# Performance work log

Hardware: AMD Instinct MI355X
Metric: run time of the kernel (lower is better)

The kernel has to match this reference:

```python
import jax, jax.numpy as jnp
import numpy as np

B, HG, WG, D, NH, K = 4, 32, 32, 768, 12, 7
HD = D // NH  # 64


def _neigh_idx(H, W, k):
    # NATTEN semantics: 7x7 window centered at the query, shifted (clamped)
    # at borders so every query has exactly k*k neighbors.
    si = np.clip(np.arange(H) - k // 2, 0, H - k)  # [H] window row starts
    sj = np.clip(np.arange(W) - k // 2, 0, W - k)  # [W] window col starts
    ri = si[:, None] + np.arange(k)[None, :]       # [H, k]
    cj = sj[:, None] + np.arange(k)[None, :]       # [W, k]
    idx = ri[:, None, :, None] * W + cj[None, :, None, :]  # [H, W, k, k]
    return jnp.asarray(idx.reshape(H * W, k * k), dtype=jnp.int32)


def setup_inputs() -> dict:
    key = jax.random.key(0)
    ks = jax.random.split(key, 3)
    s = D ** -0.5
    return {
        "x": jax.random.normal(ks[0], (B, HG * WG, D), dtype=jnp.float32),
        "qkv_w": jax.random.normal(ks[1], (3 * D, D), dtype=jnp.float32) * s,
        "qkv_b": jnp.zeros((3 * D,), dtype=jnp.float32),
        "proj_w": jax.random.normal(ks[2], (D, D), dtype=jnp.float32) * s,
        "proj_b": jnp.zeros((D,), dtype=jnp.float32),
    }


def reference(x, qkv_w, qkv_b, proj_w, proj_b):
    b, n, d = x.shape  # n == HG*WG
    idx = _neigh_idx(HG, WG, K)  # [n, K*K] flat neighbor token indices

    qkv = x @ qkv_w.T + qkv_b                      # [b, n, 3d]
    q, k, v = jnp.split(qkv, 3, axis=-1)
    q = q.reshape(b, n, NH, HD) * (HD ** -0.5)     # [b, n, h, hd]
    k = k.reshape(b, n, NH, HD)
    v = v.reshape(b, n, NH, HD)

    kn = jnp.take(k, idx, axis=1)                  # [b, n, 49, h, hd]
    vn = jnp.take(v, idx, axis=1)                  # [b, n, 49, h, hd]

    scores = jnp.einsum('bnhd,bnkhd->bnhk', q, kn)  # [b, n, h, 49]
    attn = jax.nn.softmax(scores, axis=-1)
    out = jnp.einsum('bnhk,bnkhd->bnhd', attn, vn).reshape(b, n, d)
    return out @ proj_w.T + proj_b
```

## Files before the change

kernel.cpp:

```cpp
#include <hip/hip_runtime.h>


typedef __bf16 bf16x8 __attribute__((ext_vector_type(8)));
typedef short s16x4 __attribute__((ext_vector_type(4)));
typedef float f32x4 __attribute__((ext_vector_type(4)));

__device__ __forceinline__ unsigned short f2bf(float f) {
  unsigned u = __float_as_uint(f);
  u += 0x7fffu + ((u >> 16) & 1u);
  return (unsigned short)(u >> 16);
}

template <typename T>
__device__ __forceinline__ void gld_lds16(const T* g, T* l) {
  __builtin_amdgcn_global_load_lds((const __attribute__((address_space(1))) void*)g,
                                   (__attribute__((address_space(3))) void*)l, 16, 0, 0);
}

__global__ void cvt_kernel(const float* __restrict__ x, const float* __restrict__ w1,
                           const float* __restrict__ w2, unsigned short* __restrict__ xo,
                           unsigned short* __restrict__ w1o, unsigned short* __restrict__ w2o) {
  const int n1 = 4096 * 768 / 4;
  const int n2 = 2304 * 768 / 4;
  const int n3 = 768 * 768 / 4;
  int i = blockIdx.x * 256 + threadIdx.x;
  float4 v;
  unsigned short* dst;
  int o;
  if (i < n1) {
    o = i; v = ((const float4*)x)[o]; dst = xo;
  } else if (i < n1 + n2) {
    o = i - n1; v = ((const float4*)w1)[o]; dst = w1o;
  } else if (i < n1 + n2 + n3) {
    o = i - n1 - n2; v = ((const float4*)w2)[o]; dst = w2o;
  } else {
    return;
  }
  ushort4 r;
  r.x = f2bf(v.x); r.y = f2bf(v.y); r.z = f2bf(v.z); r.w = f2bf(v.w);
  ((ushort4*)dst)[o] = r;
}

template <int MODE, int BM, int BN>
__global__ __launch_bounds__(256) void gemm_bt(const unsigned short* __restrict__ A,
                                               const unsigned short* __restrict__ Bm,
                                               const float* __restrict__ bias,
                                               unsigned short* __restrict__ obf,
                                               unsigned short* __restrict__ vtout,
                                               float* __restrict__ of32,
                                               int M, int N, int Kd) {
  constexpr int RA = BM / 64, RB = BN / 64;
  constexpr int MI = BM / 32, NI = BN / 32;
  __shared__ __align__(16) unsigned short sA[2][BM * 32];
  __shared__ __align__(16) unsigned short sB[2][BN * 32];
  const int tid = threadIdx.x;
  const int lane = tid & 63;
  const int wv = tid >> 6;

  constexpr int HX = (MODE == 0) ? 9 : 6;
  constexpr int HY = (MODE == 0) ? 8 : 16;
  const int lin = blockIdx.y * gridDim.x + blockIdx.x;
  const int xcd = lin & 7, rrr = lin >> 3;
  const int bx = (xcd & 1) * HX + rrr % HX;
  const int by = (xcd >> 1) * HY + rrr / HX;
  const int m0 = by * BM, n0 = bx * BN;

  const int wrow = (wv >> 1) * (BM / 2), wcol = (wv & 1) * (BN / 2);
  const int lr = lane & 15, lq = lane >> 4;
  const int rchunk = (lq ^ ((lr >> 1) & 3)) * 8;

  f32x4 acc[MI][NI] = {};

  const int schunk = ((tid & 3) ^ ((tid >> 3) & 3)) * 8;
  const unsigned short* gA = A + (size_t)(m0 + (tid >> 2)) * Kd + schunk;
  const unsigned short* gB = Bm + (size_t)(n0 + (tid >> 2)) * Kd + schunk;

#pragma unroll
  for (int r = 0; r < RA; ++r) gld_lds16(gA + (size_t)(r * 64) * Kd, &sA[0][r * 2048 + tid * 8]);
#pragma unroll
  for (int r = 0; r < RB; ++r) gld_lds16(gB + (size_t)(r * 64) * Kd, &sB[0][r * 2048 + tid * 8]);
  __syncthreads();

  int cur = 0;
  for (int k0 = 0; k0 < Kd; k0 += 32) {
    const int nxt = k0 + 32;
    if (nxt < Kd) {
      unsigned short* dA = sA[cur ^ 1];
      unsigned short* dB = sB[cur ^ 1];
#pragma unroll
      for (int r = 0; r < RA; ++r) gld_lds16(gA + (size_t)(r * 64) * Kd + nxt, dA + r * 2048 + tid * 8);
#pragma unroll
      for (int r = 0; r < RB; ++r) gld_lds16(gB + (size_t)(r * 64) * Kd + nxt, dB + r * 2048 + tid * 8);
    }
    const unsigned short* cA = sA[cur];
    const unsigned short* cB = sB[cur];
    bf16x8 af[MI], bfr[NI];
#pragma unroll
    for (int t = 0; t < MI; ++t) af[t] = *(const bf16x8*)(cA + (wrow + t * 16 + lr) * 32 + rchunk);
#pragma unroll
    for (int t = 0; t < NI; ++t) bfr[t] = *(const bf16x8*)(cB + (wcol + t * 16 + lr) * 32 + rchunk);
#pragma unroll
    for (int im = 0; im < MI; ++im)
#pragma unroll
      for (int in = 0; in < NI; ++in)
        acc[im][in] = __builtin_amdgcn_mfma_f32_16x16x32_bf16(af[im], bfr[in], acc[im][in], 0, 0, 0);
    __syncthreads();
    cur ^= 1;
  }

  if (MODE == 0) {
    const int sidx = n0 / 768;
    if (sidx == 2) {
#pragma unroll
      for (int im = 0; im < MI; ++im) {
#pragma unroll
        for (int in = 0; in < NI; ++in) {
          int gn = n0 + wcol + in * 16 + lr;
          int rem = gn - 1536;
          int hh = rem >> 6, dd = gn & 63;
          float bsv = bias[gn];
          int gm0 = m0 + wrow + im * 16 + lq * 4;
          ushort4 pk;
          pk.x = f2bf(acc[im][in][0] + bsv);
          pk.y = f2bf(acc[im][in][1] + bsv);
          pk.z = f2bf(acc[im][in][2] + bsv);
          pk.w = f2bf(acc[im][in][3] + bsv);
          *(ushort4*)(vtout + (size_t)(hh * 64 + dd) * 4096 + gm0) = pk;
        }
      }
    } else {
      const float scale = (sidx == 0) ? 0.18033688f : 1.0f;
#pragma unroll
      for (int im = 0; im < MI; ++im) {
#pragma unroll
        for (int in = 0; in < NI; ++in) {
          int gn = n0 + wcol + in * 16 + lr;
          int rem = gn - sidx * 768;
          int hh = rem >> 6, dd = gn & 63;
          float bsv = bias[gn];
#pragma unroll
          for (int r = 0; r < 4; ++r) {
            int gm = m0 + wrow + im * 16 + lq * 4 + r;
            float val = (acc[im][in][r] + bsv) * scale;
            obf[((size_t)(sidx * 12 + hh) * 4096 + gm) * 64 + dd] = f2bf(val);
          }
        }
      }
    }
  } else {
#pragma unroll
    for (int im = 0; im < MI; ++im) {
#pragma unroll
      for (int in = 0; in < NI; ++in) {
        int gn = n0 + wcol + in * 16 + lr;
        float bsv = bias[gn];
#pragma unroll
        for (int r = 0; r < 4; ++r) {
          int gm = m0 + wrow + im * 16 + lq * 4 + r;
          of32[(size_t)gm * N + gn] = acc[im][in][r] + bsv;
        }
      }
    }
  }
}

__global__ __launch_bounds__(256, 3) void natten_kernel(const unsigned short* __restrict__ qkvt,
                                                        unsigned short* __restrict__ aout) {
  __shared__ __align__(16) unsigned short sKV[256 * 64];
  const int h = blockIdx.x, ip = blockIdx.y, b = blockIdx.z;
  const int i0 = ip * 2;
  const int tid = threadIdx.x, lane = tid & 63, wv = tid >> 6;
  const int lg = lane >> 4, lm = lane & 15;
  int si0 = i0 - 3; si0 = si0 < 0 ? 0 : si0; if (si0 > 25) si0 = 25;
  const int gb = b * 1024;
  const unsigned short* Qg = qkvt + ((size_t)h * 4096 + gb + i0 * 32) * 64;
  const unsigned short* Kg = qkvt + ((size_t)(12 + h) * 4096 + gb) * 64;
  const unsigned short* Vg = qkvt + (size_t)24 * 4096 * 64 + (size_t)h * 64 * 4096 + gb;

  uint4 kreg[8];
#pragma unroll
  for (int it = 0; it < 8; ++it) {
    int row = si0 + it; if (row > 31) row = 31;
    kreg[it] = *(const uint4*)(Kg + (row * 32 + (tid >> 3)) * 64 + (tid & 7) * 8);
  }
  uint4 vreg[8];
#pragma unroll
  for (int it = 0; it < 8; ++it) {
    int d = it * 8 + (tid >> 5);
    int wr = (tid >> 2) & 7;
    int row = si0 + wr; if (row > 31) row = 31;
    vreg[it] = *(const uint4*)(Vg + (size_t)d * 4096 + row * 32 + (tid & 3) * 8);
  }

  const int row_sel = wv >> 1;
  const int jhalf = wv & 1;
  const int i = i0 + row_sel;
  int si_w = i - 3; si_w = si_w < 0 ? 0 : si_w; if (si_w > 25) si_w = 25;
  const int toff = (si_w - si0) * 32;
  const int j = jhalf * 16 + lm;
  int sj = j - 3; sj = sj < 0 ? 0 : sj; if (sj > 25) sj = 25;

  s16x4 qf[4];
  const int qrow = row_sel * 32 + j;
#pragma unroll
  for (int ks = 0; ks < 4; ++ks)
    qf[ks] = *(const s16x4*)(Qg + qrow * 64 + ks * 16 + lg * 4);

#pragma unroll
  for (int it = 0; it < 8; ++it) {
    int t = it * 32 + (tid >> 3);
    int c16 = tid & 7;
    int s = t & 15;
    *(uint2*)(sKV + t * 64 + ((((c16 << 1)) ^ s) << 2)) = make_uint2(kreg[it].x, kreg[it].y);
    *(uint2*)(sKV + t * 64 + ((((c16 << 1) | 1) ^ s) << 2)) = make_uint2(kreg[it].z, kreg[it].w);
  }
  __syncthreads();

  float madd[2][4];
#pragma unroll
  for (int p = 0; p < 2; ++p)
#pragma unroll
    for (int r = 0; r < 4; ++r) {
      int c = p * 16 + lg * 4 + r;
      madd[p][r] = (c >= sj && c <= sj + 6) ? 0.f : -1e30f;
    }

  f32x4 accS[14];
#pragma unroll
  for (int tt = 0; tt < 14; ++tt) {
    f32x4 a = {0.f, 0.f, 0.f, 0.f};
    const int trow = toff + tt * 16 + lm;
    const unsigned short* kr = sKV + trow * 64;
    const int sw = trow & 15;
#pragma unroll
    for (int ks = 0; ks < 4; ++ks) {
      s16x4 kf = *(const s16x4*)(kr + ((((ks << 2) + lg) ^ sw) << 2));
      a = __builtin_amdgcn_mfma_f32_16x16x16bf16_1k(kf, qf[ks], a, 0, 0, 0);
    }
    accS[tt] = a;
  }
  __syncthreads();

#pragma unroll
  for (int it = 0; it < 8; ++it) {
    int d = it * 8 + (tid >> 5);
    int tc16 = tid & 31;
    int s = d & 15;
    *(uint2*)(sKV + d * 256 + ((((tc16 << 1)) ^ s) << 2)) = make_uint2(vreg[it].x, vreg[it].y);
    *(uint2*)(sKV + d * 256 + ((((tc16 << 1) | 1) ^ s) << 2)) = make_uint2(vreg[it].z, vreg[it].w);
  }

  float mx = -3e38f;
#pragma unroll
  for (int tt = 0; tt < 14; ++tt)
#pragma unroll
    for (int r = 0; r < 4; ++r) {
      float v = accS[tt][r] + madd[tt & 1][r];
      accS[tt][r] = v;
      mx = fmaxf(mx, v);
    }
  mx = fmaxf(mx, __shfl_xor(mx, 16, 64));
  mx = fmaxf(mx, __shfl_xor(mx, 32, 64));
  float sum = 0.f;
#pragma unroll
  for (int tt = 0; tt < 14; ++tt)
#pragma unroll
    for (int r = 0; r < 4; ++r) {
      float p = exp2f(accS[tt][r] - mx);
      accS[tt][r] = p;
      sum += p;
    }
  sum += __shfl_xor(sum, 16, 64);
  sum += __shfl_xor(sum, 32, 64);
  const float inv = 1.f / sum;

  s16x4 pf[14];
#pragma unroll
  for (int tt = 0; tt < 14; ++tt) {
    union { unsigned u[2]; s16x4 v; } pk;
    pk.u[0] = ((unsigned)f2bf(accS[tt][1]) << 16) | f2bf(accS[tt][0]);
    pk.u[1] = ((unsigned)f2bf(accS[tt][3]) << 16) | f2bf(accS[tt][2]);
    pf[tt] = pk.v;
  }
  __syncthreads();

  f32x4 accO[4] = {};
  const int choff = toff >> 2;
#pragma unroll
  for (int tt = 0; tt < 14; ++tt) {
    const int c8 = choff + tt * 4 + lg;
#pragma unroll
    for (int nt = 0; nt < 4; ++nt) {
      const int d = nt * 16 + lm;
      s16x4 vf = *(const s16x4*)(sKV + d * 256 + ((c8 ^ (d & 15)) << 2));
      accO[nt] = __builtin_amdgcn_mfma_f32_16x16x16bf16_1k(pf[tt], vf, accO[nt], 0, 0, 0);
    }
  }

  float invr[4];
#pragma unroll
  for (int r = 0; r < 4; ++r) invr[r] = __shfl(inv, lg * 4 + r, 64);

  const int tokbase = gb + i * 32 + jhalf * 16;
#pragma unroll
  for (int nt = 0; nt < 4; ++nt)
#pragma unroll
    for (int r = 0; r < 4; ++r) {
      int tok = tokbase + lg * 4 + r;
      aout[(size_t)tok * 768 + h * 64 + nt * 16 + lm] = f2bf(accO[nt][r] * invr[r]);
    }
}

extern "C" void kernel_launch(void* const* d_in, const int* in_sizes, int n_in,
                              void* d_out, int out_size, void* d_ws, size_t ws_size,
                              hipStream_t stream) {
  const float* x      = (const float*)d_in[0];
  const float* qkv_w  = (const float*)d_in[1];
  const float* qkv_b  = (const float*)d_in[2];
  const float* proj_w = (const float*)d_in[3];
  const float* proj_b = (const float*)d_in[4];
  char* ws = (char*)d_ws;

  unsigned short* xb    = (unsigned short*)(ws);
  unsigned short* wqkv  = (unsigned short*)(ws + 6291456);
  unsigned short* wproj = (unsigned short*)(ws + 9830400);
  unsigned short* qkvt  = (unsigned short*)(ws + 11010048);
  unsigned short* attnb = (unsigned short*)(ws + 29884416);
  unsigned short* vt    = qkvt + (size_t)24 * 4096 * 64;
  float* out = (float*)d_out;

  cvt_kernel<<<5376, 256, 0, stream>>>(x, qkv_w, proj_w, xb, wqkv, wproj);
  gemm_bt<0, 128, 128><<<dim3(18, 32), 256, 0, stream>>>(xb, wqkv, qkv_b, qkvt, vt, nullptr, 4096, 2304, 768);
  natten_kernel<<<dim3(12, 16, 4), 256, 0, stream>>>(qkvt, attnb);
  gemm_bt<1, 64, 64><<<dim3(12, 64), 256, 0, stream>>>(attnb, wproj, proj_b, nullptr, nullptr, out, 4096, 768, 768);
}
```

Baseline: 144.1 us.

## Read K/V fragments directly from global memory in natten kernel, drop LDS staging

The natten kernel stops staging the 8-row K and V windows through shared memory with block-wide barriers. Each wave now loads its K rows and V columns straight from global memory (relying on L1/L2 caching), and QK^T switches to the 16x16x32 bf16 MFMA with 8-element fragments. This removes LDS writes, swizzling and three __syncthreads, and drops the occupancy hint in launch_bounds. The cost is redundant global/cache traffic, since waves no longer share loaded K/V and the V reads are small 8-byte strided accesses.

```diff
diff --git a/kernel.cpp b/kernel.cpp
--- a/kernel.cpp
+++ b/kernel.cpp
@@ -164,58 +164,24 @@
   }
 }
 
-__global__ __launch_bounds__(256, 3) void natten_kernel(const unsigned short* __restrict__ qkvt,
-                                                        unsigned short* __restrict__ aout) {
-  __shared__ __align__(16) unsigned short sKV[256 * 64];
+__global__ __launch_bounds__(256) void natten_kernel(const unsigned short* __restrict__ qkvt,
+                                                     unsigned short* __restrict__ aout) {
   const int h = blockIdx.x, ip = blockIdx.y, b = blockIdx.z;
   const int i0 = ip * 2;
   const int tid = threadIdx.x, lane = tid & 63, wv = tid >> 6;
   const int lg = lane >> 4, lm = lane & 15;
-  int si0 = i0 - 3; si0 = si0 < 0 ? 0 : si0; if (si0 > 25) si0 = 25;
   const int gb = b * 1024;
   const unsigned short* Qg = qkvt + ((size_t)h * 4096 + gb + i0 * 32) * 64;
   const unsigned short* Kg = qkvt + ((size_t)(12 + h) * 4096 + gb) * 64;
   const unsigned short* Vg = qkvt + (size_t)24 * 4096 * 64 + (size_t)h * 64 * 4096 + gb;
 
-  uint4 kreg[8];
-#pragma unroll
-  for (int it = 0; it < 8; ++it) {
-    int row = si0 + it; if (row > 31) row = 31;
-    kreg[it] = *(const uint4*)(Kg + (row * 32 + (tid >> 3)) * 64 + (tid & 7) * 8);
-  }
-  uint4 vreg[8];
-#pragma unroll
-  for (int it = 0; it < 8; ++it) {
-    int d = it * 8 + (tid >> 5);
-    int wr = (tid >> 2) & 7;
-    int row = si0 + wr; if (row > 31) row = 31;
-    vreg[it] = *(const uint4*)(Vg + (size_t)d * 4096 + row * 32 + (tid & 3) * 8);
-  }
-
   const int row_sel = wv >> 1;
   const int jhalf = wv & 1;
   const int i = i0 + row_sel;
   int si_w = i - 3; si_w = si_w < 0 ? 0 : si_w; if (si_w > 25) si_w = 25;
-  const int toff = (si_w - si0) * 32;
   const int j = jhalf * 16 + lm;
   int sj = j - 3; sj = sj < 0 ? 0 : sj; if (sj > 25) sj = 25;
 
-  s16x4 qf[4];
-  const int qrow = row_sel * 32 + j;
-#pragma unroll
-  for (int ks = 0; ks < 4; ++ks)
-    qf[ks] = *(const s16x4*)(Qg + qrow * 64 + ks * 16 + lg * 4);
-
-#pragma unroll
-  for (int it = 0; it < 8; ++it) {
-    int t = it * 32 + (tid >> 3);
-    int c16 = tid & 7;
-    int s = t & 15;
-    *(uint2*)(sKV + t * 64 + ((((c16 << 1)) ^ s) << 2)) = make_uint2(kreg[it].x, kreg[it].y);
-    *(uint2*)(sKV + t * 64 + ((((c16 << 1) | 1) ^ s) << 2)) = make_uint2(kreg[it].z, kreg[it].w);
-  }
-  __syncthreads();
-
   float madd[2][4];
 #pragma unroll
   for (int p = 0; p < 2; ++p)
@@ -225,29 +191,24 @@
       madd[p][r] = (c >= sj && c <= sj + 6) ? 0.f : -1e30f;
     }
 
+  bf16x8 qf[2];
+  const unsigned short* qrowp = Qg + (row_sel * 32 + j) * 64;
+#pragma unroll
+  for (int ks = 0; ks < 2; ++ks)
+    qf[ks] = *(const bf16x8*)(qrowp + ks * 32 + lg * 8);
+
+  const unsigned short* Kw = Kg + (size_t)(si_w * 32) * 64;
   f32x4 accS[14];
 #pragma unroll
   for (int tt = 0; tt < 14; ++tt) {
     f32x4 a = {0.f, 0.f, 0.f, 0.f};
-    const int trow = toff + tt * 16 + lm;
-    const unsigned short* kr = sKV + trow * 64;
-    const int sw = trow & 15;
-#pragma unroll
-    for (int ks = 0; ks < 4; ++ks) {
-      s16x4 kf = *(const s16x4*)(kr + ((((ks << 2) + lg) ^ sw) << 2));
-      a = __builtin_amdgcn_mfma_f32_16x16x16bf16_1k(kf, qf[ks], a, 0, 0, 0);
+    const unsigned short* kr = Kw + (tt * 16 + lm) * 64;
+#pragma unroll
+    for (int ks = 0; ks < 2; ++ks) {
+      bf16x8 kf = *(const bf16x8*)(kr + ks * 32 + lg * 8);
+      a = __builtin_amdgcn_mfma_f32_16x16x32_bf16(kf, qf[ks], a, 0, 0, 0);
     }
     accS[tt] = a;
-  }
-  __syncthreads();
-
-#pragma unroll
-  for (int it = 0; it < 8; ++it) {
-    int d = it * 8 + (tid >> 5);
-    int tc16 = tid & 31;
-    int s = d & 15;
-    *(uint2*)(sKV + d * 256 + ((((tc16 << 1)) ^ s) << 2)) = make_uint2(vreg[it].x, vreg[it].y);
-    *(uint2*)(sKV + d * 256 + ((((tc16 << 1) | 1) ^ s) << 2)) = make_uint2(vreg[it].z, vreg[it].w);
   }
 
   float mx = -3e38f;
@@ -282,17 +243,16 @@
     pk.u[1] = ((unsigned)f2bf(accS[tt][3]) << 16) | f2bf(accS[tt][2]);
     pf[tt] = pk.v;
   }
-  __syncthreads();
-
+
+  const unsigned short* Vw = Vg + si_w * 32;
   f32x4 accO[4] = {};
-  const int choff = toff >> 2;
 #pragma unroll
   for (int tt = 0; tt < 14; ++tt) {
-    const int c8 = choff + tt * 4 + lg;
+    const int tok4 = tt * 16 + lg * 4;
 #pragma unroll
     for (int nt = 0; nt < 4; ++nt) {
       const int d = nt * 16 + lm;
-      s16x4 vf = *(const s16x4*)(sKV + d * 256 + ((c8 ^ (d & 15)) << 2));
+      s16x4 vf = *(const s16x4*)(Vw + (size_t)d * 4096 + tok4);
       accO[nt] = __builtin_amdgcn_mfma_f32_16x16x16bf16_1k(pf[tt], vf, accO[nt], 0, 0, 0);
     }
   }
```

Result: slower. 161.4 us (+12.1%).
